# Kernel optimization log

Hardware: AMD Instinct MI355X
Metric: run time of the kernel (lower is better)

## Reference

```python
import jax, jax.numpy as jnp
import numpy as np

T, B, A, OBS = 128, 16, 32, 256
K, NACT, HID = 3, 9, 32


def setup_inputs() -> dict:
    key = jax.random.key(0)
    ks = jax.random.split(key, 12)
    sc = 0.1  # small init scale for stability
    d = {}
    d["x"] = jax.random.normal(ks[0], (T, B, A, OBS), jnp.float32)
    d["done"] = jax.random.randint(ks[1], (T, B), 0, 2, jnp.int32)
    d["actions"] = jax.random.randint(ks[2], (T, B, A, K), 0, NACT, jnp.int32)
    d["W1"] = sc * jax.random.normal(ks[3], (128, OBS), jnp.float32)
    d["b1"] = jnp.zeros((128,), jnp.float32)
    d["W2"] = sc * jax.random.normal(ks[4], (128, 128), jnp.float32)
    d["b2"] = jnp.zeros((128,), jnp.float32)
    d["W3"] = sc * jax.random.normal(ks[5], (64, 128), jnp.float32)
    d["b3"] = jnp.zeros((64,), jnp.float32)
    d["Wih"] = sc * jax.random.normal(ks[6], (4 * HID, 64), jnp.float32)
    d["Whh"] = sc * jax.random.normal(ks[7], (4 * HID, HID), jnp.float32)
    d["bih"] = jnp.zeros((4 * HID,), jnp.float32)
    d["bhh"] = jnp.zeros((4 * HID,), jnp.float32)
    d["Wh"] = sc * jax.random.normal(ks[8], (K, NACT, HID), jnp.float32)
    d["bh"] = jnp.zeros((K, NACT), jnp.float32)
    d["h0"] = jnp.zeros((B * A, HID), jnp.float32)
    d["c0"] = jnp.zeros((B * A, HID), jnp.float32)
    return d


def _forward(x, done, actions, W1, b1, W2, b2, W3, b3,
             Wih, Whh, bih, bhh, Wh, bh, h0, c0):
    # MLP trunk: n_obs -> 128 -> 128 -> 64 (tanh, tanh, linear)
    z = jnp.tanh(x @ W1.T + b1)
    z = jnp.tanh(z @ W2.T + b2)
    z = z @ W3.T + b3                       # [T, B, A, 64]
    zf = z.reshape(T, B * A, 64)
    # done[t] repeated per agent (repeat_interleave along batch*agent axis)
    done_f = jnp.repeat(done.astype(x.dtype), A, axis=1)  # [T, B*A]

    def step(carry, inp):
        h, c = carry
        zt, dt = inp                        # [B*A,64], [B*A]
        mask = (1.0 - dt)[:, None]
        h = h * mask
        c = c * mask
        gates = zt @ Wih.T + bih + h @ Whh.T + bhh  # [B*A, 4H]
        i, f, g, o = jnp.split(gates, 4, axis=-1)   # PyTorch gate order i,f,g,o
        i, f, o = jax.nn.sigmoid(i), jax.nn.sigmoid(f), jax.nn.sigmoid(o)
        g = jnp.tanh(g)
        c = f * c + i * g
        h = o * jnp.tanh(c)
        return (h, c), h

    (_, _), ys = jax.lax.scan(step, (h0, c0), (zf, done_f))
    y = ys.reshape(T, B, A, HID)
    # multi-head categorical logits: stacked heads [K, NACT, HID]
    logits = jnp.einsum('tbah,knh->tbakn', y, Wh) + bh  # [T,B,A,K,NACT]
    lp = jax.nn.log_softmax(logits, axis=-1)
    entropies = -jnp.sum(jnp.exp(lp) * lp, axis=-1)     # [T,B,A,K]
    alp = jnp.take_along_axis(lp, actions[..., None], axis=-1)[..., 0]  # [T,B,A,K]
    logprobs = jnp.prod(alp, axis=-1)  # faithful: product of per-head log-probs
    return logprobs, entropies


def reference(x, done, actions, W1, b1, W2, b2, W3, b3,
              Wih, Whh, bih, bhh, Wh, bh, h0, c0):
    logprobs, entropies = _forward(x, done, actions, W1, b1, W2, b2, W3, b3,
                                   Wih, Whh, bih, bhh, Wh, bh, h0, c0)
    return actions, logprobs, entropies
```

## Files before the change

kernel.cpp:

```cpp
#include <hip/hip_runtime.h>
#include <math.h>

namespace {
constexpr int Tn = 128, Bn = 16, An = 32, OBS = 256, Kh = 3, NACT = 9, HID = 32;
constexpr int TBA = Tn * Bn * An;
constexpr int BA  = Bn * An;
constexpr int OUT_LP  = TBA * Kh;
constexpr int OUT_ENT = TBA * Kh + TBA;
constexpr int NCHUNK = 32;
constexpr int CHUNKW = Tn / NCHUNK;

typedef __fp16   pk16x2 __attribute__((ext_vector_type(2)));
typedef _Float16 half8v __attribute__((ext_vector_type(8)));
typedef float    f32x4  __attribute__((ext_vector_type(4)));
}

__device__ __forceinline__ float fast_sig(float x) {
  return __builtin_amdgcn_rcpf(1.f + __expf(-x));
}
__device__ __forceinline__ float fast_tanh(float x) {
  return fmaf(2.f, fast_sig(2.f * x), -1.f);
}
__device__ __forceinline__ unsigned h2bits(pk16x2 h) {
  return __builtin_bit_cast(unsigned, h);
}
__device__ __forceinline__ pk16x2 bits2h(unsigned u) {
  return __builtin_bit_cast(pk16x2, u);
}
__device__ __forceinline__ int first_done_ge(unsigned long long dm0,
                                             unsigned long long dm1, int n) {
  unsigned long long m0 = (n < 64) ? (dm0 & (~0ull << n)) : 0ull;
  unsigned long long m1 = (n < 64) ? dm1 : (dm1 & (~0ull << (n - 64)));
  if (m0) return __builtin_ctzll(m0);
  if (m1) return 64 + __builtin_ctzll(m1);
  return 128;
}
__device__ __forceinline__ void bmax3(float& m0, float& m1, float& m2,
                                      int km, float v) {
  m0 = (km == 0) ? fmaxf(m0, v) : m0;
  m1 = (km == 1) ? fmaxf(m1, v) : m1;
  m2 = (km == 2) ? fmaxf(m2, v) : m2;
}
__device__ __forceinline__ void badd3(float& s0, float& s1, float& s2,
                                      int km, float v) {
  s0 += (km == 0) ? v : 0.f;
  s1 += (km == 1) ? v : 0.f;
  s2 += (km == 2) ? v : 0.f;
}
__device__ __forceinline__ float bsel3(float x0, float x1, float x2, int km) {
  return (km == 0) ? x0 : ((km == 1) ? x1 : x2);
}
__device__ __forceinline__ int bseli3(int x0, int x1, int x2, int km) {
  return (km == 0) ? x0 : ((km == 1) ? x1 : x2);
}

template<int ROWS, int WSTR>
__device__ __forceinline__ void stage_whf(const float* __restrict__ Wg, int kofs,
                                          _Float16* __restrict__ wt, int tid)
{
#pragma unroll
  for (int it = 0; it < ROWS/64; ++it) {
    int idx = tid + it*512;
    int o = idx >> 3, g8 = idx & 7;
    const float* p = &Wg[(size_t)o*WSTR + kofs + g8*8];
    float4 c0 = *(const float4*)p;
    float4 c1 = *(const float4*)(p + 4);
    half8v hv = { (_Float16)c0.x, (_Float16)c0.y, (_Float16)c0.z, (_Float16)c0.w,
                  (_Float16)c1.x, (_Float16)c1.y, (_Float16)c1.z, (_Float16)c1.w };
    *(half8v*)&wt[o*72 + g8*8] = hv;
  }
}

template<int NOC, int XSTR>
__device__ __forceinline__ void mfma_slab(const _Float16* __restrict__ xsrc,
                                          const _Float16* __restrict__ wt,
                                          int rA, int ln, int quad, f32x4 acc[8])
{
#pragma unroll
  for (int kc = 0; kc < 2; ++kc) {
    half8v a = *(const half8v*)&xsrc[rA*XSTR + kc*32 + quad*8];
#pragma unroll
    for (int oc = 0; oc < NOC; ++oc) {
      half8v b = *(const half8v*)&wt[(oc*16 + ln)*72 + kc*32 + quad*8];
      acc[oc] = __builtin_amdgcn_mfma_f32_16x16x32_f16(a, b, acc[oc], 0, 0, 0);
    }
  }
}

template<int NOC>
__device__ __forceinline__ void mfma_regA(half8v a0, half8v a1,
                                          const _Float16* __restrict__ wt,
                                          int ln, int quad, f32x4 acc[8])
{
#pragma unroll
  for (int oc = 0; oc < NOC; ++oc) {
    half8v b = *(const half8v*)&wt[(oc*16 + ln)*72 + quad*8];
    acc[oc] = __builtin_amdgcn_mfma_f32_16x16x32_f16(a0, b, acc[oc], 0, 0, 0);
  }
#pragma unroll
  for (int oc = 0; oc < NOC; ++oc) {
    half8v b = *(const half8v*)&wt[(oc*16 + ln)*72 + 32 + quad*8];
    acc[oc] = __builtin_amdgcn_mfma_f32_16x16x32_f16(a1, b, acc[oc], 0, 0, 0);
  }
}

__global__ __launch_bounds__(512, 4) void mlp_kernel(
    const float* __restrict__ x,
    const float* __restrict__ W1, const float* __restrict__ W2,
    const float* __restrict__ W3, const float* __restrict__ Wih,
    const float* __restrict__ b1, const float* __restrict__ b2,
    const float* __restrict__ b3, const float* __restrict__ bih,
    const float* __restrict__ bhh, uint2* __restrict__ G1q)
{
  __shared__ __align__(16) _Float16 wt0[128*72];
  __shared__ __align__(16) _Float16 wt1[128*72];
  __shared__ __align__(16) _Float16 act[128*136];
  const int tid  = threadIdx.x;
  const int w    = tid >> 6;
  const int lane = tid & 63;
  const int ln   = lane & 15;
  const int quad = lane >> 4;
  const int rA   = 16*w + ln;
  const int r0   = 16*w + quad*4;
  const int R0   = blockIdx.x * 128;
  f32x4 acc[8];
  const float* xrow = &x[(size_t)(R0 + rA)*OBS + quad*8];

#define XLOAD(KT, U0, U1, U2, U3) {                                   \
    const float* xp_ = xrow + (KT)*64;                                \
    U0 = *(const float4*)(xp_);      U1 = *(const float4*)(xp_ + 4);  \
    U2 = *(const float4*)(xp_ + 32); U3 = *(const float4*)(xp_ + 36); }
#define XCVT(U0, U1, U2, U3, A0, A1) {                                         \
    A0 = (half8v){(_Float16)U0.x,(_Float16)U0.y,(_Float16)U0.z,(_Float16)U0.w, \
                  (_Float16)U1.x,(_Float16)U1.y,(_Float16)U1.z,(_Float16)U1.w};\
    A1 = (half8v){(_Float16)U2.x,(_Float16)U2.y,(_Float16)U2.z,(_Float16)U2.w, \
                  (_Float16)U3.x,(_Float16)U3.y,(_Float16)U3.z,(_Float16)U3.w}; }

  float4 u0, u1, u2, u3, v0, v1, v2, v3;
  float4 y0, y1, y2, y3, z0, z1, z2, z3;
  half8v a0, a1;

  XLOAD(0, u0, u1, u2, u3);
  XLOAD(1, v0, v1, v2, v3);
  XLOAD(2, y0, y1, y2, y3);
  XLOAD(3, z0, z1, z2, z3);
  stage_whf<128, 256>(W1, 0, wt0, tid);
#pragma unroll
  for (int oc = 0; oc < 8; ++oc) acc[oc] = (f32x4)0.f;
  __syncthreads();

  stage_whf<128, 256>(W1, 64, wt1, tid);
  XCVT(u0, u1, u2, u3, a0, a1);
  mfma_regA<8>(a0, a1, wt0, ln, quad, acc);
  __syncthreads();

  stage_whf<128, 256>(W1, 128, wt0, tid);
  XCVT(v0, v1, v2, v3, a0, a1);
  mfma_regA<8>(a0, a1, wt1, ln, quad, acc);
  __syncthreads();

  stage_whf<128, 256>(W1, 192, wt1, tid);
  XCVT(y0, y1, y2, y3, a0, a1);
  mfma_regA<8>(a0, a1, wt0, ln, quad, acc);
  __syncthreads();

  stage_whf<128, 128>(W2, 0, wt0, tid);
  XCVT(z0, z1, z2, z3, a0, a1);
  mfma_regA<8>(a0, a1, wt1, ln, quad, acc);
  __syncthreads();

#pragma unroll
  for (int oc = 0; oc < 8; ++oc) {
    int o = oc*16 + ln;
    float bv = b1[o];
#pragma unroll
    for (int r = 0; r < 4; ++r)
      act[(r0 + r)*136 + o] = (_Float16)fast_tanh(acc[oc][r] + bv);
  }

#pragma unroll
  for (int oc = 0; oc < 8; ++oc) acc[oc] = (f32x4)0.f;
  stage_whf<128, 128>(W2, 64, wt1, tid);
  mfma_slab<8, 136>(act, wt0, rA, ln, quad, acc);
  __syncthreads();

  stage_whf<64, 128>(W3, 0, wt0, tid);
  mfma_slab<8, 136>(act + 64, wt1, rA, ln, quad, acc);
  __syncthreads();

#pragma unroll
  for (int oc = 0; oc < 8; ++oc) {
    int o = oc*16 + ln;
    float bv = b2[o];
#pragma unroll
    for (int r = 0; r < 4; ++r)
      act[(r0 + r)*136 + o] = (_Float16)fast_tanh(acc[oc][r] + bv);
  }

#pragma unroll
  for (int oc = 0; oc < 4; ++oc) acc[oc] = (f32x4)0.f;
  stage_whf<64, 128>(W3, 64, wt1, tid);
  mfma_slab<4, 136>(act, wt0, rA, ln, quad, acc);
  __syncthreads();

  stage_whf<128, 64>(Wih, 0, wt0, tid);
  mfma_slab<4, 136>(act + 64, wt1, rA, ln, quad, acc);
  __syncthreads();

#pragma unroll
  for (int oc = 0; oc < 4; ++oc) {
    int o = oc*16 + ln;
    float bv = b3[o];
#pragma unroll
    for (int r = 0; r < 4; ++r)
      act[(r0 + r)*136 + o] = (_Float16)(acc[oc][r] + bv);
  }

#pragma unroll
  for (int oc = 0; oc < 8; ++oc) acc[oc] = (f32x4)0.f;
  mfma_slab<8, 136>(act, wt0, rA, ln, quad, acc);
#pragma unroll
  for (int p = 0; p < 2; ++p) {
    int ui = p*16 + ln;
    float bi = bih[ui]      + bhh[ui];
    float bf = bih[ui + 32] + bhh[ui + 32];
    float bg = bih[ui + 64] + bhh[ui + 64];
    float bo = bih[ui + 96] + bhh[ui + 96];
#pragma unroll
    for (int r = 0; r < 4; ++r) {
      int n = R0 + r0 + r;
      uint2 qv;
      qv.x = h2bits(__builtin_amdgcn_cvt_pkrtz(acc[p  ][r] + bi, acc[p+4][r] + bg));
      qv.y = h2bits(__builtin_amdgcn_cvt_pkrtz(acc[p+2][r] + bf, acc[p+6][r] + bo));
      G1q[(size_t)n*32 + ui] = qv;
    }
  }
#undef XLOAD
#undef XCVT
}

__global__ __launch_bounds__(64) void lstm_kernel(
    const uint2* __restrict__ G1q, const float* __restrict__ Whh,
    const float* __restrict__ Wh, const float* __restrict__ bh,
    const int* __restrict__ done, const int* __restrict__ actions,
    const float* __restrict__ h0, const float* __restrict__ c0,
    float* __restrict__ out)
{
  static_assert(BA == 512 && NCHUNK == 32, "index math below assumes 512x32");
  const int lane = threadIdx.x;
  const int ln   = lane & 15;
  const int q    = lane >> 4;
  const int rg   = blockIdx.x & 31;
  const int ck   = blockIdx.x >> 5;
  const int R0   = rg * 16;
  const int b    = R0 >> 5;

  const unsigned long long dm0 = __ballot(done[lane*Bn + b] != 0);
  const unsigned long long dm1 = __ballot(done[(lane + 64)*Bn + b] != 0);

  const int s = (ck == 0) ? 0 : first_done_ge(dm0, dm1, ck * CHUNKW);
  const int e = (ck == NCHUNK - 1) ? Tn
                                   : first_done_ge(dm0, dm1, (ck + 1) * CHUNKW);
  if (s >= e) return;

#define WFRAG(DST, ROWBASE, SRC, STRIDE) {                                     \
    const float* p_ = &(SRC)[(size_t)((ROWBASE) + ln)*(STRIDE) + q*8];         \
    float4 c0_ = *(const float4*)p_;                                           \
    float4 c1_ = *(const float4*)(p_ + 4);                                     \
    DST = (half8v){                                                            \
      (_Float16)c0_.x, (_Float16)c0_.y, (_Float16)c0_.z, (_Float16)c0_.w,     \
      (_Float16)c1_.x, (_Float16)c1_.y, (_Float16)c1_.z, (_Float16)c1_.w}; }

  half8v wA0, wA1, wA2, wA3, wA4, wA5, wA6, wA7;
  WFRAG(wA0,   0, Whh, HID)  WFRAG(wA1,  16, Whh, HID)
  WFRAG(wA2,  32, Whh, HID)  WFRAG(wA3,  48, Whh, HID)
  WFRAG(wA4,  64, Whh, HID)  WFRAG(wA5,  80, Whh, HID)
  WFRAG(wA6,  96, Whh, HID)  WFRAG(wA7, 112, Whh, HID)

  half8v whA0, whA1;
  WFRAG(whA0, 0, Wh, HID)
  {
    int row = 16 + ln;
    int rc  = (row < 27) ? row : 0;
    float zf = (row < 27) ? 1.f : 0.f;
    const float* p_ = &Wh[(size_t)rc*HID + q*8];
    float4 c0_ = *(const float4*)p_;
    float4 c1_ = *(const float4*)(p_ + 4);
    whA1 = (half8v){
      (_Float16)(c0_.x*zf), (_Float16)(c0_.y*zf),
      (_Float16)(c0_.z*zf), (_Float16)(c0_.w*zf),
      (_Float16)(c1_.x*zf), (_Float16)(c1_.y*zf),
      (_Float16)(c1_.z*zf), (_Float16)(c1_.w*zf)};
  }
#undef WFRAG

  f32x4 bc0, bc1;
#pragma unroll
  for (int r = 0; r < 4; ++r) {
    int m0 = 4*q + r;
    int m1 = 16 + 4*q + r;
    bc0[r] = bh[m0];
    bc1[r] = (m1 < 27) ? bh[m1] : -1e30f;
  }

#define KOF(M, K, O) int K = (M)/9; K = (K > 2) ? 2 : K; const int O = (M) - 9*K;
  const int mA = 4*q, mB = 16 + 4*q;
  KOF(mA+0, kA0, oA0) KOF(mA+1, kA1, oA1) KOF(mA+2, kA2, oA2) KOF(mA+3, kA3, oA3)
  KOF(mB+0, kB0, oB0) KOF(mB+1, kB1, oB1) KOF(mB+2, kB2, oB2) KOF(mB+3, kB3, oB3)
#undef KOF

  const float4 z4 = {0.f, 0.f, 0.f, 0.f};
  float4 cs0, cs1;
  unsigned w0, w1, w2, w3;
  if (ck == 0) {
    const float* hp = &h0[(size_t)(R0 + ln)*HID + 4*q];
    const float* cp = &c0[(size_t)(R0 + ln)*HID + 4*q];
    float4 ha = *(const float4*)hp;
    float4 hb = *(const float4*)(hp + 16);
    cs0 = *(const float4*)cp;
    cs1 = *(const float4*)(cp + 16);
    w0 = h2bits(__builtin_amdgcn_cvt_pkrtz(ha.x, ha.y));
    w1 = h2bits(__builtin_amdgcn_cvt_pkrtz(ha.z, ha.w));
    w2 = h2bits(__builtin_amdgcn_cvt_pkrtz(hb.x, hb.y));
    w3 = h2bits(__builtin_amdgcn_cvt_pkrtz(hb.z, hb.w));
  } else {
    cs0 = z4; cs1 = z4;
    w0 = w1 = w2 = w3 = 0u;
  }

  const int aA = (ln + ((q & 1) << 5)) << 2;
  const int aB = aA + (16 << 2);
  const bool loq = (q < 2);

#define BBUILD(DST) {                                                      \
    unsigned e0_ = (unsigned)__builtin_amdgcn_ds_bpermute(aA, (int)w0);    \
    unsigned e1_ = (unsigned)__builtin_amdgcn_ds_bpermute(aA, (int)w1);    \
    unsigned e2_ = (unsigned)__builtin_amdgcn_ds_bpermute(aA, (int)w2);    \
    unsigned e3_ = (unsigned)__builtin_amdgcn_ds_bpermute(aA, (int)w3);    \
    unsigned o0_ = (unsigned)__builtin_amdgcn_ds_bpermute(aB, (int)w0);    \
    unsigned o1_ = (unsigned)__builtin_amdgcn_ds_bpermute(aB, (int)w1);    \
    unsigned o2_ = (unsigned)__builtin_amdgcn_ds_bpermute(aB, (int)w2);    \
    unsigned o3_ = (unsigned)__builtin_amdgcn_ds_bpermute(aB, (int)w3);    \
    uint4 bu_;                                                             \
    bu_.x = loq ? e0_ : e2_;  bu_.y = loq ? e1_ : e3_;                     \
    bu_.z = loq ? o0_ : o2_;  bu_.w = loq ? o1_ : o3_;                     \
    DST = __builtin_bit_cast(half8v, bu_); }

  half8v Bprev;
  if (ck == 0) { BBUILD(Bprev) }
  else {
    uint4 zz; zz.x = zz.y = zz.z = zz.w = 0u;
    Bprev = __builtin_bit_cast(half8v, zz);
  }

  const uint2* gb = G1q + ((size_t)(R0 + ln) * 32 + 4*q);
  const size_t gstep = (size_t)BA * 32;

#define LOADG(T, A0, A1, A2, A3)                                  \
  { const uint2* p_ = gb + (size_t)(T) * gstep;                   \
    A0 = *(const uint4*)(p_);      A1 = *(const uint4*)(p_ + 2);  \
    A2 = *(const uint4*)(p_ + 16); A3 = *(const uint4*)(p_ + 18); }

  uint4 rc0, rc1, rc2, rc3;
  LOADG(s, rc0, rc1, rc2, rc3);

  for (int t = s; t < e; ++t) {
    int tn = (t + 1 < e) ? t + 1 : e - 1;
    uint4 rn0, rn1, rn2, rn3;
    LOADG(tn, rn0, rn1, rn2, rn3);

    const int rowG = t*BA + R0 + ln;
    const int* ap = actions + (size_t)rowG*3;
    int a0 = ap[0], a1 = ap[1], a2 = ap[2];

    unsigned long long dbit = (t < 64) ? (dm0 >> t) : (dm1 >> (t - 64));
    half8v Buse = Bprev;
    if (dbit & 1ull) {
      uint4 zz; zz.x = zz.y = zz.z = zz.w = 0u;
      Buse = __builtin_bit_cast(half8v, zz);
      cs0 = z4; cs1 = z4;
    }

    f32x4 ci0, cf0, cg0, co0, ci1, cf1, cg1, co1;
    {
      pk16x2 ig, fo;
      ig = bits2h(rc0.x); fo = bits2h(rc0.y);
      ci0[0] = ig.x; cg0[0] = ig.y; cf0[0] = fo.x; co0[0] = fo.y;
      ig = bits2h(rc0.z); fo = bits2h(rc0.w);
      ci0[1] = ig.x; cg0[1] = ig.y; cf0[1] = fo.x; co0[1] = fo.y;
      ig = bits2h(rc1.x); fo = bits2h(rc1.y);
      ci0[2] = ig.x; cg0[2] = ig.y; cf0[2] = fo.x; co0[2] = fo.y;
      ig = bits2h(rc1.z); fo = bits2h(rc1.w);
      ci0[3] = ig.x; cg0[3] = ig.y; cf0[3] = fo.x; co0[3] = fo.y;
      ig = bits2h(rc2.x); fo = bits2h(rc2.y);
      ci1[0] = ig.x; cg1[0] = ig.y; cf1[0] = fo.x; co1[0] = fo.y;
      ig = bits2h(rc2.z); fo = bits2h(rc2.w);
      ci1[1] = ig.x; cg1[1] = ig.y; cf1[1] = fo.x; co1[1] = fo.y;
      ig = bits2h(rc3.x); fo = bits2h(rc3.y);
      ci1[2] = ig.x; cg1[2] = ig.y; cf1[2] = fo.x; co1[2] = fo.y;
      ig = bits2h(rc3.z); fo = bits2h(rc3.w);
      ci1[3] = ig.x; cg1[3] = ig.y; cf1[3] = fo.x; co1[3] = fo.y;
    }

    f32x4 ai0 = __builtin_amdgcn_mfma_f32_16x16x32_f16(wA0, Buse, ci0, 0, 0, 0);
    f32x4 ai1 = __builtin_amdgcn_mfma_f32_16x16x32_f16(wA1, Buse, ci1, 0, 0, 0);
    f32x4 af0 = __builtin_amdgcn_mfma_f32_16x16x32_f16(wA2, Buse, cf0, 0, 0, 0);
    f32x4 af1 = __builtin_amdgcn_mfma_f32_16x16x32_f16(wA3, Buse, cf1, 0, 0, 0);
    f32x4 ag0 = __builtin_amdgcn_mfma_f32_16x16x32_f16(wA4, Buse, cg0, 0, 0, 0);
    f32x4 ag1 = __builtin_amdgcn_mfma_f32_16x16x32_f16(wA5, Buse, cg1, 0, 0, 0);
    f32x4 ao0 = __builtin_amdgcn_mfma_f32_16x16x32_f16(wA6, Buse, co0, 0, 0, 0);
    f32x4 ao1 = __builtin_amdgcn_mfma_f32_16x16x32_f16(wA7, Buse, co1, 0, 0, 0);

    f32x4 hva, hvb;
#pragma unroll
    for (int r = 0; r < 4; ++r) {
      float iv = fast_sig(ai0[r]);
      float fv = fast_sig(af0[r]);
      float gv = fast_tanh(ag0[r]);
      float ov = fast_sig(ao0[r]);
      float cc = fmaf(fv, cs0[r], iv * gv);
      cs0[r] = cc;
      hva[r] = ov * fast_tanh(cc);
    }
#pragma unroll
    for (int r = 0; r < 4; ++r) {
      float iv = fast_sig(ai1[r]);
      float fv = fast_sig(af1[r]);
      float gv = fast_tanh(ag1[r]);
      float ov = fast_sig(ao1[r]);
      float cc = fmaf(fv, cs1[r], iv * gv);
      cs1[r] = cc;
      hvb[r] = ov * fast_tanh(cc);
    }

    w0 = h2bits(__builtin_amdgcn_cvt_pkrtz(hva[0], hva[1]));
    w1 = h2bits(__builtin_amdgcn_cvt_pkrtz(hva[2], hva[3]));
    w2 = h2bits(__builtin_amdgcn_cvt_pkrtz(hvb[0], hvb[1]));
    w3 = h2bits(__builtin_amdgcn_cvt_pkrtz(hvb[2], hvb[3]));
    BBUILD(Bprev)

    f32x4 lh0 = __builtin_amdgcn_mfma_f32_16x16x32_f16(whA0, Bprev, bc0, 0, 0, 0);
    f32x4 lh1 = __builtin_amdgcn_mfma_f32_16x16x32_f16(whA1, Bprev, bc1, 0, 0, 0);

    float mx0 = -1e30f, mx1 = -1e30f, mx2 = -1e30f;
    bmax3(mx0, mx1, mx2, kA0, lh0[0]); bmax3(mx0, mx1, mx2, kA1, lh0[1]);
    bmax3(mx0, mx1, mx2, kA2, lh0[2]); bmax3(mx0, mx1, mx2, kA3, lh0[3]);
    bmax3(mx0, mx1, mx2, kB0, lh1[0]); bmax3(mx0, mx1, mx2, kB1, lh1[1]);
    bmax3(mx0, mx1, mx2, kB2, lh1[2]); bmax3(mx0, mx1, mx2, kB3, lh1[3]);
    mx0 = fmaxf(mx0, __shfl_xor(mx0, 16)); mx0 = fmaxf(mx0, __shfl_xor(mx0, 32));
    mx1 = fmaxf(mx1, __shfl_xor(mx1, 16)); mx1 = fmaxf(mx1, __shfl_xor(mx1, 32));
    mx2 = fmaxf(mx2, __shfl_xor(mx2, 16)); mx2 = fmaxf(mx2, __shfl_xor(mx2, 32));

    float ev0 = __expf(lh0[0] - bsel3(mx0, mx1, mx2, kA0));
    float ev1 = __expf(lh0[1] - bsel3(mx0, mx1, mx2, kA1));
    float ev2 = __expf(lh0[2] - bsel3(mx0, mx1, mx2, kA2));
    float ev3 = __expf(lh0[3] - bsel3(mx0, mx1, mx2, kA3));
    float ev4 = __expf(lh1[0] - bsel3(mx0, mx1, mx2, kB0));
    float ev5 = __expf(lh1[1] - bsel3(mx0, mx1, mx2, kB1));
    float ev6 = __expf(lh1[2] - bsel3(mx0, mx1, mx2, kB2));
    float ev7 = __expf(lh1[3] - bsel3(mx0, mx1, mx2, kB3));
    float s0 = 0.f, s1 = 0.f, s2 = 0.f;
    badd3(s0, s1, s2, kA0, ev0); badd3(s0, s1, s2, kA1, ev1);
    badd3(s0, s1, s2, kA2, ev2); badd3(s0, s1, s2, kA3, ev3);
    badd3(s0, s1, s2, kB0, ev4); badd3(s0, s1, s2, kB1, ev5);
    badd3(s0, s1, s2, kB2, ev6); badd3(s0, s1, s2, kB3, ev7);
    s0 += __shfl_xor(s0, 16); s0 += __shfl_xor(s0, 32);
    s1 += __shfl_xor(s1, 16); s1 += __shfl_xor(s1, 32);
    s2 += __shfl_xor(s2, 16); s2 += __shfl_xor(s2, 32);
    float lse0 = mx0 + __logf(s0);
    float lse1 = mx1 + __logf(s1);
    float lse2 = mx2 + __logf(s2);
    float sc0 = __expf(mx0 - lse0);
    float sc1 = __expf(mx1 - lse1);
    float sc2 = __expf(mx2 - lse2);

    float en0 = 0.f, en1 = 0.f, en2 = 0.f;
    float pl = 1.f;
#define HSLOT(LV, EV, KM, OM) {                                \
      float lse_ = bsel3(lse0, lse1, lse2, KM);                \
      float lp_  = (LV) - lse_;                                \
      float p_   = (EV) * bsel3(sc0, sc1, sc2, KM);            \
      badd3(en0, en1, en2, KM, -p_ * lp_);                     \
      int a_ = bseli3(a0, a1, a2, KM);                         \
      pl = ((OM) == a_) ? pl * lp_ : pl; }
    HSLOT(lh0[0], ev0, kA0, oA0) HSLOT(lh0[1], ev1, kA1, oA1)
    HSLOT(lh0[2], ev2, kA2, oA2) HSLOT(lh0[3], ev3, kA3, oA3)
    HSLOT(lh1[0], ev4, kB0, oB0) HSLOT(lh1[1], ev5, kB1, oB1)
    HSLOT(lh1[2], ev6, kB2, oB2) HSLOT(lh1[3], ev7, kB3, oB3)
#undef HSLOT
    en0 += __shfl_xor(en0, 16); en0 += __shfl_xor(en0, 32);
    en1 += __shfl_xor(en1, 16); en1 += __shfl_xor(en1, 32);
    en2 += __shfl_xor(en2, 16); en2 += __shfl_xor(en2, 32);
    pl  *= __shfl_xor(pl, 16);  pl  *= __shfl_xor(pl, 32);

    if (q == 0) {
      float* ob = out + (size_t)rowG*3;
      ob[0] = (float)a0; ob[1] = (float)a1; ob[2] = (float)a2;
      float* eb = out + OUT_ENT + (size_t)rowG*3;
      eb[0] = en0; eb[1] = en1; eb[2] = en2;
      out[OUT_LP + rowG] = pl;
    }

    rc0 = rn0; rc1 = rn1; rc2 = rn2; rc3 = rn3;
  }
#undef LOADG
#undef BBUILD
}

extern "C" void kernel_launch(void* const* d_in, const int* in_sizes, int n_in,
                              void* d_out, int out_size, void* d_ws, size_t ws_size,
                              hipStream_t stream)
{
  const float* x       = (const float*)d_in[0];
  const int*   done    = (const int*)  d_in[1];
  const int*   actions = (const int*)  d_in[2];
  const float* W1  = (const float*)d_in[3];
  const float* b1  = (const float*)d_in[4];
  const float* W2  = (const float*)d_in[5];
  const float* b2  = (const float*)d_in[6];
  const float* W3  = (const float*)d_in[7];
  const float* b3  = (const float*)d_in[8];
  const float* Wih = (const float*)d_in[9];
  const float* Whh = (const float*)d_in[10];
  const float* bih = (const float*)d_in[11];
  const float* bhh = (const float*)d_in[12];
  const float* Wh  = (const float*)d_in[13];
  const float* bh  = (const float*)d_in[14];
  const float* h0  = (const float*)d_in[15];
  const float* c0  = (const float*)d_in[16];
  float* out = (float*)d_out;

  uint2* G1q = (uint2*)d_ws;

  mlp_kernel<<<TBA/128, 512, 0, stream>>>(
      x, W1, W2, W3, Wih, b1, b2, b3, bih, bhh, G1q);
  lstm_kernel<<<32 * NCHUNK, 64, 0, stream>>>(
      G1q, Whh, Wh, bh, done, actions, h0, c0, out);
}
```

Baseline: 168.9 us.

## Load MLP weight fragments directly from global memory instead of LDS staging

The MLP kernel no longer copies W1/W2/W3/Wih into shared-memory tiles. Each wave now reads its MFMA B-fragments straight from global memory and converts them to fp16 in registers, which removes every __syncthreads. The x prefetch depth also drops from four k-tiles to two, to save registers. This cuts LDS usage and barrier stalls, which may raise occupancy, but every wave now fetches and converts the full weight set on its own, adding redundant L1/L2 traffic and conversion work.

```diff
diff --git a/kernel.cpp b/kernel.cpp
--- a/kernel.cpp
+++ b/kernel.cpp
@@ -54,54 +54,13 @@
   return (km == 0) ? x0 : ((km == 1) ? x1 : x2);
 }
 
-template<int ROWS, int WSTR>
-__device__ __forceinline__ void stage_whf(const float* __restrict__ Wg, int kofs,
-                                          _Float16* __restrict__ wt, int tid)
-{
-#pragma unroll
-  for (int it = 0; it < ROWS/64; ++it) {
-    int idx = tid + it*512;
-    int o = idx >> 3, g8 = idx & 7;
-    const float* p = &Wg[(size_t)o*WSTR + kofs + g8*8];
-    float4 c0 = *(const float4*)p;
-    float4 c1 = *(const float4*)(p + 4);
-    half8v hv = { (_Float16)c0.x, (_Float16)c0.y, (_Float16)c0.z, (_Float16)c0.w,
-                  (_Float16)c1.x, (_Float16)c1.y, (_Float16)c1.z, (_Float16)c1.w };
-    *(half8v*)&wt[o*72 + g8*8] = hv;
-  }
-}
-
-template<int NOC, int XSTR>
-__device__ __forceinline__ void mfma_slab(const _Float16* __restrict__ xsrc,
-                                          const _Float16* __restrict__ wt,
-                                          int rA, int ln, int quad, f32x4 acc[8])
-{
-#pragma unroll
-  for (int kc = 0; kc < 2; ++kc) {
-    half8v a = *(const half8v*)&xsrc[rA*XSTR + kc*32 + quad*8];
-#pragma unroll
-    for (int oc = 0; oc < NOC; ++oc) {
-      half8v b = *(const half8v*)&wt[(oc*16 + ln)*72 + kc*32 + quad*8];
-      acc[oc] = __builtin_amdgcn_mfma_f32_16x16x32_f16(a, b, acc[oc], 0, 0, 0);
-    }
-  }
-}
-
-template<int NOC>
-__device__ __forceinline__ void mfma_regA(half8v a0, half8v a1,
-                                          const _Float16* __restrict__ wt,
-                                          int ln, int quad, f32x4 acc[8])
-{
-#pragma unroll
-  for (int oc = 0; oc < NOC; ++oc) {
-    half8v b = *(const half8v*)&wt[(oc*16 + ln)*72 + quad*8];
-    acc[oc] = __builtin_amdgcn_mfma_f32_16x16x32_f16(a0, b, acc[oc], 0, 0, 0);
-  }
-#pragma unroll
-  for (int oc = 0; oc < NOC; ++oc) {
-    half8v b = *(const half8v*)&wt[(oc*16 + ln)*72 + 32 + quad*8];
-    acc[oc] = __builtin_amdgcn_mfma_f32_16x16x32_f16(a1, b, acc[oc], 0, 0, 0);
-  }
+__device__ __forceinline__ half8v wfrag(const float* __restrict__ Wg,
+                                        int stride, int o, int kbase) {
+  const float* p = &Wg[(size_t)o*stride + kbase];
+  float4 c0 = *(const float4*)p;
+  float4 c1 = *(const float4*)(p + 4);
+  return (half8v){(_Float16)c0.x, (_Float16)c0.y, (_Float16)c0.z, (_Float16)c0.w,
+                  (_Float16)c1.x, (_Float16)c1.y, (_Float16)c1.z, (_Float16)c1.w};
 }
 
 __global__ __launch_bounds__(512, 4) void mlp_kernel(
@@ -112,8 +71,6 @@
     const float* __restrict__ b3, const float* __restrict__ bih,
     const float* __restrict__ bhh, uint2* __restrict__ G1q)
 {
-  __shared__ __align__(16) _Float16 wt0[128*72];
-  __shared__ __align__(16) _Float16 wt1[128*72];
   __shared__ __align__(16) _Float16 act[128*136];
   const int tid  = threadIdx.x;
   const int w    = tid >> 6;
@@ -136,38 +93,42 @@
     A1 = (half8v){(_Float16)U2.x,(_Float16)U2.y,(_Float16)U2.z,(_Float16)U2.w, \
                   (_Float16)U3.x,(_Float16)U3.y,(_Float16)U3.z,(_Float16)U3.w}; }
 
+#define MM_REGA(NOC, WG, WSTR, KB, A0, A1)                                  \
+  _Pragma("unroll") for (int oc = 0; oc < (NOC); ++oc) {                    \
+    half8v b_ = wfrag(WG, WSTR, oc*16 + ln, (KB) + quad*8);                 \
+    acc[oc] = __builtin_amdgcn_mfma_f32_16x16x32_f16(A0, b_, acc[oc],0,0,0);\
+  }                                                                         \
+  _Pragma("unroll") for (int oc = 0; oc < (NOC); ++oc) {                    \
+    half8v b_ = wfrag(WG, WSTR, oc*16 + ln, (KB) + 32 + quad*8);            \
+    acc[oc] = __builtin_amdgcn_mfma_f32_16x16x32_f16(A1, b_, acc[oc],0,0,0);\
+  }
+
+#define MM_ACT(NOC, WG, WSTR, KB)                                              \
+  _Pragma("unroll") for (int kc = 0; kc < 2; ++kc) {                           \
+    half8v a_ = *(const half8v*)&act[rA*136 + (KB) + kc*32 + quad*8];          \
+    _Pragma("unroll") for (int oc = 0; oc < (NOC); ++oc) {                     \
+      half8v b_ = wfrag(WG, WSTR, oc*16 + ln, (KB) + kc*32 + quad*8);          \
+      acc[oc] = __builtin_amdgcn_mfma_f32_16x16x32_f16(a_, b_, acc[oc],0,0,0); \
+    }                                                                          \
+  }
+
   float4 u0, u1, u2, u3, v0, v1, v2, v3;
-  float4 y0, y1, y2, y3, z0, z1, z2, z3;
   half8v a0, a1;
 
+#pragma unroll
+  for (int oc = 0; oc < 8; ++oc) acc[oc] = (f32x4)0.f;
   XLOAD(0, u0, u1, u2, u3);
   XLOAD(1, v0, v1, v2, v3);
-  XLOAD(2, y0, y1, y2, y3);
-  XLOAD(3, z0, z1, z2, z3);
-  stage_whf<128, 256>(W1, 0, wt0, tid);
-#pragma unroll
-  for (int oc = 0; oc < 8; ++oc) acc[oc] = (f32x4)0.f;
-  __syncthreads();
-
-  stage_whf<128, 256>(W1, 64, wt1, tid);
   XCVT(u0, u1, u2, u3, a0, a1);
-  mfma_regA<8>(a0, a1, wt0, ln, quad, acc);
-  __syncthreads();
-
-  stage_whf<128, 256>(W1, 128, wt0, tid);
+  MM_REGA(8, W1, 256, 0, a0, a1)
+  XLOAD(2, u0, u1, u2, u3);
   XCVT(v0, v1, v2, v3, a0, a1);
-  mfma_regA<8>(a0, a1, wt1, ln, quad, acc);
-  __syncthreads();
-
-  stage_whf<128, 256>(W1, 192, wt1, tid);
-  XCVT(y0, y1, y2, y3, a0, a1);
-  mfma_regA<8>(a0, a1, wt0, ln, quad, acc);
-  __syncthreads();
-
-  stage_whf<128, 128>(W2, 0, wt0, tid);
-  XCVT(z0, z1, z2, z3, a0, a1);
-  mfma_regA<8>(a0, a1, wt1, ln, quad, acc);
-  __syncthreads();
+  MM_REGA(8, W1, 256, 64, a0, a1)
+  XLOAD(3, v0, v1, v2, v3);
+  XCVT(u0, u1, u2, u3, a0, a1);
+  MM_REGA(8, W1, 256, 128, a0, a1)
+  XCVT(v0, v1, v2, v3, a0, a1);
+  MM_REGA(8, W1, 256, 192, a0, a1)
 
 #pragma unroll
   for (int oc = 0; oc < 8; ++oc) {
@@ -180,14 +141,8 @@
 
 #pragma unroll
   for (int oc = 0; oc < 8; ++oc) acc[oc] = (f32x4)0.f;
-  stage_whf<128, 128>(W2, 64, wt1, tid);
-  mfma_slab<8, 136>(act, wt0, rA, ln, quad, acc);
-  __syncthreads();
-
-  stage_whf<64, 128>(W3, 0, wt0, tid);
-  mfma_slab<8, 136>(act + 64, wt1, rA, ln, quad, acc);
-  __syncthreads();
-
+  MM_ACT(8, W2, 128, 0)
+  MM_ACT(8, W2, 128, 64)
 #pragma unroll
   for (int oc = 0; oc < 8; ++oc) {
     int o = oc*16 + ln;
@@ -199,14 +154,8 @@
 
 #pragma unroll
   for (int oc = 0; oc < 4; ++oc) acc[oc] = (f32x4)0.f;
-  stage_whf<64, 128>(W3, 64, wt1, tid);
-  mfma_slab<4, 136>(act, wt0, rA, ln, quad, acc);
-  __syncthreads();
-
-  stage_whf<128, 64>(Wih, 0, wt0, tid);
-  mfma_slab<4, 136>(act + 64, wt1, rA, ln, quad, acc);
-  __syncthreads();
-
+  MM_ACT(4, W3, 128, 0)
+  MM_ACT(4, W3, 128, 64)
 #pragma unroll
   for (int oc = 0; oc < 4; ++oc) {
     int o = oc*16 + ln;
@@ -218,7 +167,7 @@
 
 #pragma unroll
   for (int oc = 0; oc < 8; ++oc) acc[oc] = (f32x4)0.f;
-  mfma_slab<8, 136>(act, wt0, rA, ln, quad, acc);
+  MM_ACT(8, Wih, 64, 0)
 #pragma unroll
   for (int p = 0; p < 2; ++p) {
     int ui = p*16 + ln;
@@ -237,6 +186,8 @@
   }
 #undef XLOAD
 #undef XCVT
+#undef MM_REGA
+#undef MM_ACT
 }
 
 __global__ __launch_bounds__(64) void lstm_kernel(
```

Result: slower. 264.1 us (+56.4%).
